# Optimization experiments

Hardware: AMD Instinct MI355X
Metric: run time of the kernel (lower is better)

The kernel has to match this reference:

```python
import jax, jax.numpy as jnp
from jax import lax
import numpy as np

T, IN, H, L = 8192, 128, 1024, 3


def setup_inputs() -> dict:
    key = jax.random.key(0)
    ks = jax.random.split(key, 12)
    s = 0.05  # scale params to avoid saturating sigmoid/tanh
    return {
        "S": jax.random.normal(ks[0], (T, IN), jnp.float32),
        "h0": jax.random.normal(ks[1], (L, H), jnp.float32),
        "w_ih0": jax.random.normal(ks[2], (2 * H, IN), jnp.float32) * s,
        "w_hh0": jax.random.normal(ks[3], (2 * H, H), jnp.float32) * s,
        "b_ih0": jax.random.normal(ks[4], (2 * H,), jnp.float32) * s,
        "b_hh0": jax.random.normal(ks[5], (2 * H,), jnp.float32) * s,
        "w_ih_rest": jax.random.normal(ks[6], (L - 1, 2 * H, H), jnp.float32) * s,
        "w_hh_rest": jax.random.normal(ks[7], (L - 1, 2 * H, H), jnp.float32) * s,
        "b_ih_rest": jax.random.normal(ks[8], (L - 1, 2 * H), jnp.float32) * s,
        "b_hh_rest": jax.random.normal(ks[9], (L - 1, 2 * H), jnp.float32) * s,
        "w_out": jax.random.normal(ks[10], (1, H), jnp.float32) * s,
        "b_out": jax.random.normal(ks[11], (1,), jnp.float32) * s,
    }


def _mgu_layer(x_seq, h0, w_ih, w_hh, b_ih, b_hh):
    # Precompute the input projection for all timesteps at once: [T, 2H]
    gi = x_seq @ w_ih.T + b_ih

    def step(h, gi_t):
        gh = h @ w_hh.T + b_hh                      # [2H]
        i_f, i_n = jnp.split(gi_t, 2)
        h_f, h_n = jnp.split(gh, 2)
        f = jax.nn.sigmoid(i_f + h_f)               # forget gate
        n = jnp.tanh(i_n + f * h_n)                 # new candidate
        hy = n + (1.0 - f) * (h - n)
        return hy, hy

    _, out = lax.scan(step, h0, gi)                 # out: [T, H]
    return out


def reference(S, h0, w_ih0, w_hh0, b_ih0, b_hh0,
              w_ih_rest, w_hh_rest, b_ih_rest, b_hh_rest,
              w_out, b_out):
    x = _mgu_layer(S, h0[0], w_ih0, w_hh0, b_ih0, b_hh0)
    for l in range(w_ih_rest.shape[0]):             # fixed small layer count
        x = _mgu_layer(x, h0[l + 1], w_ih_rest[l], w_hh_rest[l],
                       b_ih_rest[l], b_hh_rest[l])
    out = (x @ w_out.T + b_out).reshape(-1)          # [T]
    return out
```

## Files before the change

kernel.cpp:

```cpp
#include <hip/hip_runtime.h>
#include <math.h>
#include <stdint.h>


#define T_STEPS 8192
#define HDIM 1024
#define RING 128
#define SLACK (RING - 16)

typedef unsigned long long u64;

__device__ __forceinline__ u64 agload64(const u64* p) {
    return __hip_atomic_load(p, __ATOMIC_RELAXED, __HIP_MEMORY_SCOPE_AGENT);
}
__device__ __forceinline__ void agstore64(u64* p, u64 v) {
    __hip_atomic_store(p, v, __ATOMIC_RELAXED, __HIP_MEMORY_SCOPE_AGENT);
}
__device__ __forceinline__ int agloadi(const int* p) {
    return __hip_atomic_load(p, __ATOMIC_RELAXED, __HIP_MEMORY_SCOPE_AGENT);
}
__device__ __forceinline__ void agstorei(int* p, int v) {
    __hip_atomic_store(p, v, __ATOMIC_RELAXED, __HIP_MEMORY_SCOPE_AGENT);
}
__device__ __forceinline__ float dot4(float4 a, float4 b) {
    return a.x * b.x + a.y * b.y + a.z * b.z + a.w * b.w;
}
__device__ __forceinline__ u64 pack(float v, int tag) {
    return ((u64)(unsigned)tag << 32) | (u64)__float_as_uint(v);
}
__device__ __forceinline__ void opaque4(float4& v) {
    asm volatile("" : "+v"(v.x), "+v"(v.y), "+v"(v.z), "+v"(v.w));
}
__device__ __forceinline__ void opaque2(float2& v) {
    asm volatile("" : "+v"(v.x), "+v"(v.y));
}

__device__ __forceinline__ int minscan64(const int* parr, int q) {
    int p = agloadi(parr + q);
#pragma unroll
    for (int off = 32; off; off >>= 1) {
        const int o = __shfl_xor(p, off, 64);
        p = p < o ? p : o;
    }
    return p;
}

template <int L>
__device__ void rec_layer(float* __restrict__ s_h,
                          float* __restrict__ s_x0,
                          float (*__restrict__ s_gi)[16],
                          const float* __restrict__ S,
                          const float* __restrict__ h0,
                          const float* __restrict__ w_ih,
                          const float* __restrict__ b_ih,
                          const float* __restrict__ w_hh,
                          const float* __restrict__ b_hh,
                          const u64* __restrict__ giRing,
                          u64* __restrict__ ring_out,
                          float* __restrict__ xout,
                          u64* __restrict__ htag,
                          const int* __restrict__ progArr,
                          int* __restrict__ progGiSelf,
                          int r)
{
    const int tid = threadIdx.x;
    const int a   = tid >> 6;
    const int q   = tid & 63;
    const int jb  = r * 8 + 2 * a;

    float4 wf[2][4], wn[2][4];
#pragma unroll
    for (int g = 0; g < 2; ++g) {
        const float* rf = w_hh + (size_t)(jb + g) * HDIM;
        const float* rn = w_hh + (size_t)(HDIM + jb + g) * HDIM;
#pragma unroll
        for (int m = 0; m < 4; ++m) {
            wf[g][m] = *(const float4*)(rf + 4 * q + 256 * m);
            wn[g][m] = *(const float4*)(rn + 4 * q + 256 * m);
            opaque4(wf[g][m]); opaque4(wn[g][m]);
        }
    }
    float2 wif2[2] = {}, win2[2] = {};
    float bFv[2], bInv[2] = {0.f, 0.f}, bHnv[2];
    if constexpr (L == 0) {
#pragma unroll
        for (int g = 0; g < 2; ++g) {
            wif2[g] = *(const float2*)(w_ih + (size_t)(jb + g) * 128 + 2 * q);
            win2[g] = *(const float2*)(w_ih + (size_t)(HDIM + jb + g) * 128 + 2 * q);
            opaque2(wif2[g]); opaque2(win2[g]);
            bFv[g]  = b_ih[jb + g] + b_hh[jb + g];
            bInv[g] = b_ih[HDIM + jb + g];
            bHnv[g] = b_hh[HDIM + jb + g];
        }
    } else {
#pragma unroll
        for (int g = 0; g < 2; ++g) {
            bFv[g]  = b_hh[jb + g];
            bHnv[g] = b_hh[HDIM + jb + g];
        }
    }

    int lastProg = 0;

    for (int t = 0; t < T_STEPS; ++t) {
        const int par = t & 1;
        float* hD = s_h + par * HDIM;
        const u64* hrow = htag + (size_t)((t + 1) & 1) * HDIM;
        u64*       hpub = htag + (size_t)par * HDIM;

        if constexpr (L < 2) {
            if (t - lastProg > SLACK) {
                do { lastProg = minscan64(progArr, q); }
                while (t - lastProg > SLACK);
            }
        }

        if constexpr (L == 0) {
            float* xD = s_x0 + par * 128;
            if (tid < 32)
                ((float4*)xD)[tid] = ((const float4*)(S + (size_t)t * 128))[tid];
        } else {
            if (tid < 16) {
                const unsigned xe = (unsigned)(t + 1);
                const u64* p = giRing + (size_t)(t & (RING - 1)) * 2048
                             + (tid < 8 ? (size_t)(8 * r + tid)
                                        : (size_t)(1024 + 8 * r + (tid - 8)));
                u64 w;
                do { w = agload64(p); } while ((unsigned)(w >> 32) != xe);
                s_gi[par][tid] = __uint_as_float((unsigned)w);
            }
        }

        if (t == 0) {
            hD[tid]       = h0[tid];
            hD[tid + 256] = h0[tid + 256];
            hD[tid + 512] = h0[tid + 512];
            hD[tid + 768] = h0[tid + 768];
        } else {
            const unsigned he = (unsigned)t;
            u64 w0 = 0, w1 = 0, w2 = 0, w3 = 0;
            bool d0 = false, d1 = false, d2 = false, d3 = false;
            while (!(d0 && d1 && d2 && d3)) {
                if (!d0) { w0 = agload64(hrow + tid);       d0 = ((unsigned)(w0 >> 32) == he); }
                if (!d1) { w1 = agload64(hrow + tid + 256); d1 = ((unsigned)(w1 >> 32) == he); }
                if (!d2) { w2 = agload64(hrow + tid + 512); d2 = ((unsigned)(w2 >> 32) == he); }
                if (!d3) { w3 = agload64(hrow + tid + 768); d3 = ((unsigned)(w3 >> 32) == he); }
            }
            hD[tid]       = __uint_as_float((unsigned)w0);
            hD[tid + 256] = __uint_as_float((unsigned)w1);
            hD[tid + 512] = __uint_as_float((unsigned)w2);
            hD[tid + 768] = __uint_as_float((unsigned)w3);
        }
        __syncthreads();

        if constexpr (L > 0) {
            if (r == 0 && tid == 0) agstorei(progGiSelf, t + 1);
        }

        float aF[2]  = {0.f, 0.f};
        float aNh[2] = {0.f, 0.f};
        float aNi[2] = {0.f, 0.f};
#pragma unroll
        for (int m = 0; m < 4; ++m) {
            const float4 h4 = ((const float4*)hD)[q + 64 * m];
#pragma unroll
            for (int g = 0; g < 2; ++g) {
                aF[g]  += dot4(wf[g][m], h4);
                aNh[g] += dot4(wn[g][m], h4);
            }
        }
        if constexpr (L == 0) {
            const float* xD = s_x0 + par * 128;
            const float2 x2 = *(const float2*)&xD[2 * q];
#pragma unroll
            for (int g = 0; g < 2; ++g) {
                aF[g]  += wif2[g].x * x2.x + wif2[g].y * x2.y;
                aNi[g] += win2[g].x * x2.x + win2[g].y * x2.y;
            }
        }

#pragma unroll
        for (int g = 0; g < 2; ++g) {
            aF[g]  += __shfl_xor(aF[g],  1, 64);
            aNh[g] += __shfl_xor(aNh[g], 1, 64);
            if constexpr (L == 0) aNi[g] += __shfl_xor(aNi[g], 1, 64);
        }
        const int gsl = q & 1;
        float vF  = gsl ? aF[1]  : aF[0];
        float vNh = gsl ? aNh[1] : aNh[0];
        float vNi = 0.f;
        if constexpr (L == 0) vNi = gsl ? aNi[1] : aNi[0];
#pragma unroll
        for (int off = 2; off <= 32; off <<= 1) {
            vF  += __shfl_xor(vF,  off, 64);
            vNh += __shfl_xor(vNh, off, 64);
            if constexpr (L == 0) vNi += __shfl_xor(vNi, off, 64);
        }

        if (q < 2) {
            const int   j  = jb + q;
            const float hp = hD[j];
            float f, n;
            if constexpr (L == 0) {
                const float cF  = gsl ? bFv[1]  : bFv[0];
                const float cIn = gsl ? bInv[1] : bInv[0];
                const float cHn = gsl ? bHnv[1] : bHnv[0];
                f = 1.f / (1.f + expf(-(vF + cF)));
                n = tanhf(vNi + cIn + f * (vNh + cHn));
            } else {
                const float cHf = gsl ? bFv[1]  : bFv[0];
                const float cHn = gsl ? bHnv[1] : bHnv[0];
                const float gf  = s_gi[par][2 * a + q];
                const float gn  = s_gi[par][8 + 2 * a + q];
                f = 1.f / (1.f + expf(-(gf + vF + cHf)));
                n = tanhf(gn + f * (vNh + cHn));
            }
            const float hy = n + (1.f - f) * (hp - n);
            const u64   pk = pack(hy, t + 1);
            agstore64(hpub + j, pk);
            if constexpr (L < 2) {
                agstore64(ring_out + (size_t)(t & (RING - 1)) * HDIM + j, pk);
            } else {
                xout[(size_t)t * HDIM + j] = hy;
            }
        }
    }
}

__device__ void army_layer(float* __restrict__ s_x,
                           const u64* __restrict__ xring,
                           u64* __restrict__ giRing,
                           const float* __restrict__ w_ih,
                           const float* __restrict__ b_ih,
                           const int* __restrict__ progGiNext,
                           int* __restrict__ progSelf,
                           int r)
{
    const int tid = threadIdx.x;
    const int a   = tid >> 6;
    const int q   = tid & 63;
    const int jb  = r * 16 + 4 * a;

    float4 wiF[4][4], wiN[4][4];
#pragma unroll
    for (int g = 0; g < 4; ++g) {
        const float* rf = w_ih + (size_t)(jb + g) * HDIM;
        const float* rn = w_ih + (size_t)(HDIM + jb + g) * HDIM;
#pragma unroll
        for (int m = 0; m < 4; ++m) {
            wiF[g][m] = *(const float4*)(rf + 4 * q + 256 * m);
            wiN[g][m] = *(const float4*)(rn + 4 * q + 256 * m);
            opaque4(wiF[g][m]); opaque4(wiN[g][m]);
        }
    }
    float bIF[4], bIN[4];
#pragma unroll
    for (int g = 0; g < 4; ++g) {
        bIF[g] = b_ih[jb + g];
        bIN[g] = b_ih[HDIM + jb + g];
    }

    int lastProg = 0;

    for (int t = 0; t < T_STEPS; ++t) {
        const int par = t & 1;
        float* xD = s_x + par * HDIM;

        if (t - lastProg > SLACK) {
            do { lastProg = agloadi(progGiNext); } while (t - lastProg > SLACK);
        }

        {
            const unsigned xe = (unsigned)(t + 1);
            const u64* xrow = xring + (size_t)(t & (RING - 1)) * HDIM;
            u64 w0 = 0, w1 = 0, w2 = 0, w3 = 0;
            bool d0 = false, d1 = false, d2 = false, d3 = false;
            while (!(d0 && d1 && d2 && d3)) {
                if (!d0) { w0 = agload64(xrow + tid);       d0 = ((unsigned)(w0 >> 32) == xe); }
                if (!d1) { w1 = agload64(xrow + tid + 256); d1 = ((unsigned)(w1 >> 32) == xe); }
                if (!d2) { w2 = agload64(xrow + tid + 512); d2 = ((unsigned)(w2 >> 32) == xe); }
                if (!d3) { w3 = agload64(xrow + tid + 768); d3 = ((unsigned)(w3 >> 32) == xe); }
            }
            xD[tid]       = __uint_as_float((unsigned)w0);
            xD[tid + 256] = __uint_as_float((unsigned)w1);
            xD[tid + 512] = __uint_as_float((unsigned)w2);
            xD[tid + 768] = __uint_as_float((unsigned)w3);
        }
        __syncthreads();

        if (tid == 0) agstorei(progSelf, t + 1);

        float aGF[4] = {0.f, 0.f, 0.f, 0.f};
        float aGN[4] = {0.f, 0.f, 0.f, 0.f};
#pragma unroll
        for (int m = 0; m < 4; ++m) {
            const float4 x4 = ((const float4*)xD)[q + 64 * m];
#pragma unroll
            for (int g = 0; g < 4; ++g) {
                aGF[g] += dot4(wiF[g][m], x4);
                aGN[g] += dot4(wiN[g][m], x4);
            }
        }

#pragma unroll
        for (int g = 0; g < 4; ++g) {
            aGF[g] += __shfl_xor(aGF[g], 1, 64);
            aGN[g] += __shfl_xor(aGN[g], 1, 64);
        }
        const int s1 = q & 1;
        float bF0 = s1 ? aGF[1] : aGF[0];
        float bF1 = s1 ? aGF[3] : aGF[2];
        float bN0 = s1 ? aGN[1] : aGN[0];
        float bN1 = s1 ? aGN[3] : aGN[2];
        bF0 += __shfl_xor(bF0, 2, 64);
        bF1 += __shfl_xor(bF1, 2, 64);
        bN0 += __shfl_xor(bN0, 2, 64);
        bN1 += __shfl_xor(bN1, 2, 64);
        const int s2 = (q >> 1) & 1;
        float vGF = s2 ? bF1 : bF0;
        float vGN = s2 ? bN1 : bN0;
#pragma unroll
        for (int off = 4; off <= 32; off <<= 1) {
            vGF += __shfl_xor(vGF, off, 64);
            vGN += __shfl_xor(vGN, off, 64);
        }

        if (q < 4) {
            const int j = jb + q;
            u64* grow = giRing + (size_t)(t & (RING - 1)) * 2048;
            const float bf = s1 ? (s2 ? bIF[3] : bIF[1]) : (s2 ? bIF[2] : bIF[0]);
            const float bn = s1 ? (s2 ? bIN[3] : bIN[1]) : (s2 ? bIN[2] : bIN[0]);
            agstore64(grow + j,        pack(vGF + bf, t + 1));
            agstore64(grow + 1024 + j, pack(vGN + bn, t + 1));
        }
    }
}

__global__ __launch_bounds__(256, 2)
void mgu_pipe(const float* __restrict__ S,
              const float* __restrict__ h0,
              const float* __restrict__ w_ih0, const float* __restrict__ b_ih0,
              const float* __restrict__ w_hh0, const float* __restrict__ b_hh0,
              const float* __restrict__ w_ih_r, const float* __restrict__ b_ih_r,
              const float* __restrict__ w_hh_r, const float* __restrict__ b_hh_r,
              float* __restrict__ xbuf2, u64* __restrict__ ring0,
              u64* __restrict__ ring1, u64* __restrict__ gi1,
              u64* __restrict__ gi2, u64* __restrict__ htag,
              int* __restrict__ prog)
{
    __shared__ __align__(16) float s_h[2 * HDIM];
    __shared__ __align__(16) float s_x0[2 * 128];
    __shared__ float s_gi[2][16];

    int* prog_gi1 = prog + 0;
    int* prog_gi2 = prog + 16;
    int* prog_a3  = prog + 64;
    int* prog_a4  = prog + 128;

    const int bid = blockIdx.x;
    if (bid < 128) {
        rec_layer<0>(s_h, s_x0, s_gi, S, h0,
                     w_ih0, b_ih0, w_hh0, b_hh0,
                     nullptr, ring0, nullptr,
                     htag, prog_a3, nullptr, bid);
    } else if (bid < 256) {
        rec_layer<1>(s_h, nullptr, s_gi, nullptr, h0 + HDIM,
                     nullptr, nullptr, w_hh_r, b_hh_r,
                     gi1, ring1, nullptr,
                     htag + 2 * HDIM, prog_a4, prog_gi1, bid - 128);
    } else if (bid < 384) {
        rec_layer<2>(s_h, nullptr, s_gi, nullptr, h0 + 2 * HDIM,
                     nullptr, nullptr, w_hh_r + 2048 * 1024, b_hh_r + 2048,
                     gi2, nullptr, xbuf2,
                     htag + 4 * HDIM, nullptr, prog_gi2, bid - 256);
    } else if (bid < 448) {
        army_layer(s_h, ring0, gi1, w_ih_r, b_ih_r,
                   prog_gi1, prog_a3 + (bid - 384), bid - 384);
    } else {
        army_layer(s_h, ring1, gi2, w_ih_r + 2048 * 1024, b_ih_r + 2048,
                   prog_gi2, prog_a4 + (bid - 448), bid - 448);
    }
}

__global__ __launch_bounds__(256)
void mgu_out(const float* __restrict__ x,
             const float* __restrict__ w_out,
             const float* __restrict__ b_out,
             float* __restrict__ out)
{
    const int wave = threadIdx.x >> 6;
    const int lane = threadIdx.x & 63;
    const int t = blockIdx.x * 4 + wave;
    float acc = 0.f;
#pragma unroll
    for (int m = 0; m < 4; ++m) {
        const int i4 = lane + 64 * m;
        const float4 x4 = ((const float4*)(x + (size_t)t * HDIM))[i4];
        const float4 w4 = ((const float4*)w_out)[i4];
        acc += dot4(x4, w4);
    }
#pragma unroll
    for (int off = 32; off > 0; off >>= 1) acc += __shfl_xor(acc, off, 64);
    if (lane == 0) out[t] = acc + b_out[0];
}

extern "C" void kernel_launch(void* const* d_in, const int* in_sizes, int n_in,
                              void* d_out, int out_size, void* d_ws, size_t ws_size,
                              hipStream_t stream) {
    const float* S      = (const float*)d_in[0];
    const float* h0     = (const float*)d_in[1];
    const float* w_ih0  = (const float*)d_in[2];
    const float* w_hh0  = (const float*)d_in[3];
    const float* b_ih0  = (const float*)d_in[4];
    const float* b_hh0  = (const float*)d_in[5];
    const float* w_ih_r = (const float*)d_in[6];
    const float* w_hh_r = (const float*)d_in[7];
    const float* b_ih_r = (const float*)d_in[8];
    const float* b_hh_r = (const float*)d_in[9];
    const float* w_out  = (const float*)d_in[10];
    const float* b_out  = (const float*)d_in[11];
    float* out = (float*)d_out;

    char* ws = (char*)d_ws;
    float* xbuf2 = (float*)(ws);
    u64*   ring0 = (u64*)(ws + (32u << 20));
    u64*   ring1 = (u64*)(ws + (33u << 20));
    u64*   gi1   = (u64*)(ws + (34u << 20));
    u64*   gi2   = (u64*)(ws + (36u << 20));
    u64*   htag  = (u64*)(ws + (38u << 20));
    int*   prog  = (int*)(ws + (38u << 20) + (64u << 10));

    mgu_pipe<<<512, 256, 0, stream>>>(S, h0, w_ih0, b_ih0, w_hh0, b_hh0,
                                      w_ih_r, b_ih_r, w_hh_r, b_hh_r,
                                      xbuf2, ring0, ring1, gi1, gi2,
                                      htag, prog);
    mgu_out<<<2048, 256, 0, stream>>>(xbuf2, w_out, b_out, out);
}
```

Baseline: 25.07 ms.

## Repartition MGU pipeline to 512-thread blocks, 32 per layer, with sc0 polling

Each block now uses 512 threads, and blocks are interleaved by role (blockIdx & 7) so each recurrent layer runs on 32 blocks instead of 128. Each wave now computes 4 hidden units, so the per-step all-to-all h exchange has fewer participants and the progress scans cover 32 entries. The h polling uses inline-asm sc0 loads with a spin-count fallback to agent-scope atomics, and the h publish stores twice with sc0 and sc1. The gi ring load is issued before the h poll to overlap it. This risks higher per-block latency from the larger blocks and depends on cache-coherence bits that are not documented here.

```diff
diff --git a/kernel.cpp b/kernel.cpp
--- a/kernel.cpp
+++ b/kernel.cpp
@@ -7,6 +7,7 @@
 #define HDIM 1024
 #define RING 128
 #define SLACK (RING - 16)
+#define HSPIN_FB 3000
 
 typedef unsigned long long u64;
 
@@ -35,8 +36,24 @@
     asm volatile("" : "+v"(v.x), "+v"(v.y));
 }
 
-__device__ __forceinline__ int minscan64(const int* parr, int q) {
-    int p = agloadi(parr + q);
+__device__ __forceinline__ void poll2_sc0(u64& w0, u64& w1,
+                                          const u64* p0, const u64* p1) {
+    asm volatile("global_load_dwordx2 %0, %2, off sc0\n\t"
+                 "global_load_dwordx2 %1, %3, off sc0\n\t"
+                 "s_waitcnt vmcnt(0)"
+                 : "=&v"(w0), "=&v"(w1)
+                 : "v"(p0), "v"(p1)
+                 : "memory");
+    __builtin_amdgcn_sched_barrier(0);
+}
+__device__ __forceinline__ void pub_dual(u64* p, u64 v) {
+    asm volatile("global_store_dwordx2 %0, %1, off sc0\n\t"
+                 "global_store_dwordx2 %0, %1, off sc1"
+                 :: "v"(p), "v"(v) : "memory");
+}
+
+__device__ __forceinline__ int minscan32(const int* parr, int q) {
+    int p = agloadi(parr + (q & 31));
 #pragma unroll
     for (int off = 32; off; off >>= 1) {
         const int o = __shfl_xor(p, off, 64);
@@ -48,7 +65,7 @@
 template <int L>
 __device__ void rec_layer(float* __restrict__ s_h,
                           float* __restrict__ s_x0,
-                          float (*__restrict__ s_gi)[16],
+                          float (*__restrict__ s_gi)[64],
                           const float* __restrict__ S,
                           const float* __restrict__ h0,
                           const float* __restrict__ w_ih,
@@ -66,11 +83,11 @@
     const int tid = threadIdx.x;
     const int a   = tid >> 6;
     const int q   = tid & 63;
-    const int jb  = r * 8 + 2 * a;
-
-    float4 wf[2][4], wn[2][4];
-#pragma unroll
-    for (int g = 0; g < 2; ++g) {
+    const int jb  = r * 32 + 4 * a;
+
+    float4 wf[4][4], wn[4][4];
+#pragma unroll
+    for (int g = 0; g < 4; ++g) {
         const float* rf = w_hh + (size_t)(jb + g) * HDIM;
         const float* rn = w_hh + (size_t)(HDIM + jb + g) * HDIM;
 #pragma unroll
@@ -80,27 +97,25 @@
             opaque4(wf[g][m]); opaque4(wn[g][m]);
         }
     }
-    float2 wif2[2] = {}, win2[2] = {};
-    float bFv[2], bInv[2] = {0.f, 0.f}, bHnv[2];
-    if constexpr (L == 0) {
-#pragma unroll
-        for (int g = 0; g < 2; ++g) {
+    float2 wif2[4] = {}, win2[4] = {};
+    float bFv[4], bInv[4] = {}, bHnv[4];
+#pragma unroll
+    for (int g = 0; g < 4; ++g) {
+        if constexpr (L == 0) {
             wif2[g] = *(const float2*)(w_ih + (size_t)(jb + g) * 128 + 2 * q);
             win2[g] = *(const float2*)(w_ih + (size_t)(HDIM + jb + g) * 128 + 2 * q);
             opaque2(wif2[g]); opaque2(win2[g]);
             bFv[g]  = b_ih[jb + g] + b_hh[jb + g];
             bInv[g] = b_ih[HDIM + jb + g];
             bHnv[g] = b_hh[HDIM + jb + g];
-        }
-    } else {
-#pragma unroll
-        for (int g = 0; g < 2; ++g) {
+        } else {
             bFv[g]  = b_hh[jb + g];
             bHnv[g] = b_hh[HDIM + jb + g];
         }
     }
 
-    int lastProg = 0;
+    int  lastProg = 0;
+    bool hslow    = false;
 
     for (int t = 0; t < T_STEPS; ++t) {
         const int par = t & 1;
@@ -110,46 +125,63 @@
 
         if constexpr (L < 2) {
             if (t - lastProg > SLACK) {
-                do { lastProg = minscan64(progArr, q); }
+                do { lastProg = minscan32(progArr, q); }
                 while (t - lastProg > SLACK);
             }
         }
 
-        if constexpr (L == 0) {
-            float* xD = s_x0 + par * 128;
+        float4 sv;
+        u64 gw = 0; const u64* gp = nullptr;
+        if constexpr (L == 0) {
             if (tid < 32)
-                ((float4*)xD)[tid] = ((const float4*)(S + (size_t)t * 128))[tid];
+                sv = ((const float4*)(S + (size_t)t * 128))[tid];
         } else {
-            if (tid < 16) {
-                const unsigned xe = (unsigned)(t + 1);
-                const u64* p = giRing + (size_t)(t & (RING - 1)) * 2048
-                             + (tid < 8 ? (size_t)(8 * r + tid)
-                                        : (size_t)(1024 + 8 * r + (tid - 8)));
-                u64 w;
-                do { w = agload64(p); } while ((unsigned)(w >> 32) != xe);
-                s_gi[par][tid] = __uint_as_float((unsigned)w);
+            if (tid < 64) {
+                gp = giRing + (size_t)(t & (RING - 1)) * 2048
+                   + (tid < 32 ? (size_t)(32 * r + tid)
+                               : (size_t)(1024 + 32 * r + (tid - 32)));
+                gw = agload64(gp);
             }
         }
 
         if (t == 0) {
             hD[tid]       = h0[tid];
-            hD[tid + 256] = h0[tid + 256];
             hD[tid + 512] = h0[tid + 512];
-            hD[tid + 768] = h0[tid + 768];
         } else {
             const unsigned he = (unsigned)t;
-            u64 w0 = 0, w1 = 0, w2 = 0, w3 = 0;
-            bool d0 = false, d1 = false, d2 = false, d3 = false;
-            while (!(d0 && d1 && d2 && d3)) {
-                if (!d0) { w0 = agload64(hrow + tid);       d0 = ((unsigned)(w0 >> 32) == he); }
-                if (!d1) { w1 = agload64(hrow + tid + 256); d1 = ((unsigned)(w1 >> 32) == he); }
-                if (!d2) { w2 = agload64(hrow + tid + 512); d2 = ((unsigned)(w2 >> 32) == he); }
-                if (!d3) { w3 = agload64(hrow + tid + 768); d3 = ((unsigned)(w3 >> 32) == he); }
-            }
-            hD[tid]       = __uint_as_float((unsigned)w0);
-            hD[tid + 256] = __uint_as_float((unsigned)w1);
-            hD[tid + 512] = __uint_as_float((unsigned)w2);
-            hD[tid + 768] = __uint_as_float((unsigned)w3);
+            const u64* p0 = hrow + tid;
+            const u64* p1 = hrow + tid + 512;
+            u64 hw0 = 0, hw1 = 0;
+            bool done = false;
+            if (!hslow) {
+                int spins = 0;
+                for (;;) {
+                    poll2_sc0(hw0, hw1, p0, p1);
+                    if ((unsigned)(hw0 >> 32) == he &&
+                        (unsigned)(hw1 >> 32) == he) { done = true; break; }
+                    if (++spins > HSPIN_FB) { hslow = true; break; }
+                }
+            }
+            if (!done) {
+                bool d0 = ((unsigned)(hw0 >> 32) == he);
+                bool d1 = ((unsigned)(hw1 >> 32) == he);
+                while (!(d0 && d1)) {
+                    if (!d0) { hw0 = agload64(p0); d0 = ((unsigned)(hw0 >> 32) == he); }
+                    if (!d1) { hw1 = agload64(p1); d1 = ((unsigned)(hw1 >> 32) == he); }
+                }
+            }
+            hD[tid]       = __uint_as_float((unsigned)hw0);
+            hD[tid + 512] = __uint_as_float((unsigned)hw1);
+        }
+
+        if constexpr (L == 0) {
+            if (tid < 32) ((float4*)(s_x0 + par * 128))[tid] = sv;
+        } else {
+            if (tid < 64) {
+                const unsigned xe = (unsigned)(t + 1);
+                while ((unsigned)(gw >> 32) != xe) gw = agload64(gp);
+                s_gi[par][tid] = __uint_as_float((unsigned)gw);
+            }
         }
         __syncthreads();
 
@@ -157,14 +189,14 @@
             if (r == 0 && tid == 0) agstorei(progGiSelf, t + 1);
         }
 
-        float aF[2]  = {0.f, 0.f};
-        float aNh[2] = {0.f, 0.f};
-        float aNi[2] = {0.f, 0.f};
+        float aF[4]  = {};
+        float aNh[4] = {};
+        float aNi[4] = {};
 #pragma unroll
         for (int m = 0; m < 4; ++m) {
             const float4 h4 = ((const float4*)hD)[q + 64 * m];
 #pragma unroll
-            for (int g = 0; g < 2; ++g) {
+            for (int g = 0; g < 4; ++g) {
                 aF[g]  += dot4(wf[g][m], h4);
                 aNh[g] += dot4(wn[g][m], h4);
             }
@@ -173,51 +205,67 @@
             const float* xD = s_x0 + par * 128;
             const float2 x2 = *(const float2*)&xD[2 * q];
 #pragma unroll
-            for (int g = 0; g < 2; ++g) {
+            for (int g = 0; g < 4; ++g) {
                 aF[g]  += wif2[g].x * x2.x + wif2[g].y * x2.y;
                 aNi[g] += win2[g].x * x2.x + win2[g].y * x2.y;
             }
         }
 
 #pragma unroll
-        for (int g = 0; g < 2; ++g) {
+        for (int g = 0; g < 4; ++g) {
             aF[g]  += __shfl_xor(aF[g],  1, 64);
             aNh[g] += __shfl_xor(aNh[g], 1, 64);
             if constexpr (L == 0) aNi[g] += __shfl_xor(aNi[g], 1, 64);
         }
-        const int gsl = q & 1;
-        float vF  = gsl ? aF[1]  : aF[0];
-        float vNh = gsl ? aNh[1] : aNh[0];
+        const int s1 = q & 1;
+        float fF0  = s1 ? aF[1]  : aF[0];
+        float fF1  = s1 ? aF[3]  : aF[2];
+        float fNh0 = s1 ? aNh[1] : aNh[0];
+        float fNh1 = s1 ? aNh[3] : aNh[2];
+        float fNi0 = 0.f, fNi1 = 0.f;
+        if constexpr (L == 0) {
+            fNi0 = s1 ? aNi[1] : aNi[0];
+            fNi1 = s1 ? aNi[3] : aNi[2];
+        }
+        fF0  += __shfl_xor(fF0,  2, 64);
+        fF1  += __shfl_xor(fF1,  2, 64);
+        fNh0 += __shfl_xor(fNh0, 2, 64);
+        fNh1 += __shfl_xor(fNh1, 2, 64);
+        if constexpr (L == 0) {
+            fNi0 += __shfl_xor(fNi0, 2, 64);
+            fNi1 += __shfl_xor(fNi1, 2, 64);
+        }
+        const int s2 = (q >> 1) & 1;
+        float vF  = s2 ? fF1  : fF0;
+        float vNh = s2 ? fNh1 : fNh0;
         float vNi = 0.f;
-        if constexpr (L == 0) vNi = gsl ? aNi[1] : aNi[0];
-#pragma unroll
-        for (int off = 2; off <= 32; off <<= 1) {
+        if constexpr (L == 0) vNi = s2 ? fNi1 : fNi0;
+#pragma unroll
+        for (int off = 4; off <= 32; off <<= 1) {
             vF  += __shfl_xor(vF,  off, 64);
             vNh += __shfl_xor(vNh, off, 64);
             if constexpr (L == 0) vNi += __shfl_xor(vNi, off, 64);
         }
 
-        if (q < 2) {
+        if (q < 4) {
             const int   j  = jb + q;
             const float hp = hD[j];
+            const float cF  = s1 ? (s2 ? bFv[3]  : bFv[1])  : (s2 ? bFv[2]  : bFv[0]);
+            const float cHn = s1 ? (s2 ? bHnv[3] : bHnv[1]) : (s2 ? bHnv[2] : bHnv[0]);
             float f, n;
             if constexpr (L == 0) {
-                const float cF  = gsl ? bFv[1]  : bFv[0];
-                const float cIn = gsl ? bInv[1] : bInv[0];
-                const float cHn = gsl ? bHnv[1] : bHnv[0];
+                const float cIn = s1 ? (s2 ? bInv[3] : bInv[1]) : (s2 ? bInv[2] : bInv[0]);
                 f = 1.f / (1.f + expf(-(vF + cF)));
                 n = tanhf(vNi + cIn + f * (vNh + cHn));
             } else {
-                const float cHf = gsl ? bFv[1]  : bFv[0];
-                const float cHn = gsl ? bHnv[1] : bHnv[0];
-                const float gf  = s_gi[par][2 * a + q];
-                const float gn  = s_gi[par][8 + 2 * a + q];
-                f = 1.f / (1.f + expf(-(gf + vF + cHf)));
+                const float gf = s_gi[par][4 * a + q];
+                const float gn = s_gi[par][32 + 4 * a + q];
+                f = 1.f / (1.f + expf(-(gf + vF + cF)));
                 n = tanhf(gn + f * (vNh + cHn));
             }
             const float hy = n + (1.f - f) * (hp - n);
             const u64   pk = pack(hy, t + 1);
-            agstore64(hpub + j, pk);
+            pub_dual(hpub + j, pk);
             if constexpr (L < 2) {
                 agstore64(ring_out + (size_t)(t & (RING - 1)) * HDIM + j, pk);
             } else {
@@ -239,7 +287,7 @@
     const int tid = threadIdx.x;
     const int a   = tid >> 6;
     const int q   = tid & 63;
-    const int jb  = r * 16 + 4 * a;
+    const int jb  = r * 32 + 4 * a;
 
     float4 wiF[4][4], wiN[4][4];
 #pragma unroll
@@ -273,25 +321,21 @@
         {
             const unsigned xe = (unsigned)(t + 1);
             const u64* xrow = xring + (size_t)(t & (RING - 1)) * HDIM;
-            u64 w0 = 0, w1 = 0, w2 = 0, w3 = 0;
-            bool d0 = false, d1 = false, d2 = false, d3 = false;
-            while (!(d0 && d1 && d2 && d3)) {
+            u64 w0 = 0, w1 = 0;
+            bool d0 = false, d1 = false;
+            while (!(d0 && d1)) {
                 if (!d0) { w0 = agload64(xrow + tid);       d0 = ((unsigned)(w0 >> 32) == xe); }
-                if (!d1) { w1 = agload64(xrow + tid + 256); d1 = ((unsigned)(w1 >> 32) == xe); }
-                if (!d2) { w2 = agload64(xrow + tid + 512); d2 = ((unsigned)(w2 >> 32) == xe); }
-                if (!d3) { w3 = agload64(xrow + tid + 768); d3 = ((unsigned)(w3 >> 32) == xe); }
+                if (!d1) { w1 = agload64(xrow + tid + 512); d1 = ((unsigned)(w1 >> 32) == xe); }
             }
             xD[tid]       = __uint_as_float((unsigned)w0);
-            xD[tid + 256] = __uint_as_float((unsigned)w1);
-            xD[tid + 512] = __uint_as_float((unsigned)w2);
-            xD[tid + 768] = __uint_as_float((unsigned)w3);
+            xD[tid + 512] = __uint_as_float((unsigned)w1);
         }
         __syncthreads();
 
         if (tid == 0) agstorei(progSelf, t + 1);
 
-        float aGF[4] = {0.f, 0.f, 0.f, 0.f};
-        float aGN[4] = {0.f, 0.f, 0.f, 0.f};
+        float aGF[4] = {};
+        float aGN[4] = {};
 #pragma unroll
         for (int m = 0; m < 4; ++m) {
             const float4 x4 = ((const float4*)xD)[q + 64 * m];
@@ -336,7 +380,7 @@
     }
 }
 
-__global__ __launch_bounds__(256, 2)
+__global__ __launch_bounds__(512, 2)
 void mgu_pipe(const float* __restrict__ S,
               const float* __restrict__ h0,
               const float* __restrict__ w_ih0, const float* __restrict__ b_ih0,
@@ -350,35 +394,38 @@
 {
     __shared__ __align__(16) float s_h[2 * HDIM];
     __shared__ __align__(16) float s_x0[2 * 128];
-    __shared__ float s_gi[2][16];
+    __shared__ float s_gi[2][64];
 
     int* prog_gi1 = prog + 0;
     int* prog_gi2 = prog + 16;
-    int* prog_a3  = prog + 64;
-    int* prog_a4  = prog + 128;
-
-    const int bid = blockIdx.x;
-    if (bid < 128) {
+    int* prog_a1  = prog + 64;
+    int* prog_a2  = prog + 128;
+
+    const int role = blockIdx.x & 7;
+    const int r    = blockIdx.x >> 3;
+    if (r >= 32) return;
+
+    if (role == 0) {
         rec_layer<0>(s_h, s_x0, s_gi, S, h0,
                      w_ih0, b_ih0, w_hh0, b_hh0,
                      nullptr, ring0, nullptr,
-                     htag, prog_a3, nullptr, bid);
-    } else if (bid < 256) {
+                     htag, prog_a1, nullptr, r);
+    } else if (role == 1) {
         rec_layer<1>(s_h, nullptr, s_gi, nullptr, h0 + HDIM,
                      nullptr, nullptr, w_hh_r, b_hh_r,
                      gi1, ring1, nullptr,
-                     htag + 2 * HDIM, prog_a4, prog_gi1, bid - 128);
-    } else if (bid < 384) {
+                     htag + 2 * HDIM, prog_a2, prog_gi1, r);
+    } else if (role == 2) {
         rec_layer<2>(s_h, nullptr, s_gi, nullptr, h0 + 2 * HDIM,
                      nullptr, nullptr, w_hh_r + 2048 * 1024, b_hh_r + 2048,
                      gi2, nullptr, xbuf2,
-                     htag + 4 * HDIM, nullptr, prog_gi2, bid - 256);
-    } else if (bid < 448) {
+                     htag + 4 * HDIM, nullptr, prog_gi2, r);
+    } else if (role == 3) {
         army_layer(s_h, ring0, gi1, w_ih_r, b_ih_r,
-                   prog_gi1, prog_a3 + (bid - 384), bid - 384);
-    } else {
+                   prog_gi1, prog_a1 + r, r);
+    } else if (role == 4) {
         army_layer(s_h, ring1, gi2, w_ih_r + 2048 * 1024, b_ih_r + 2048,
-                   prog_gi2, prog_a4 + (bid - 448), bid - 448);
+                   prog_gi2, prog_a2 + r, r);
     }
 }
 
@@ -430,7 +477,7 @@
     u64*   htag  = (u64*)(ws + (38u << 20));
     int*   prog  = (int*)(ws + (38u << 20) + (64u << 10));
 
-    mgu_pipe<<<512, 256, 0, stream>>>(S, h0, w_ih0, b_ih0, w_hh0, b_hh0,
+    mgu_pipe<<<512, 512, 0, stream>>>(S, h0, w_ih0, b_ih0, w_hh0, b_hh0,
                                       w_ih_r, b_ih_r, w_hh_r, b_hh_r,
                                       xbuf2, ring0, ring1, gi1, gi2,
                                       htag, prog);
```

Result: slower. 38.50 ms (+53.6%).

## Repartition persistent MGU pipeline into fewer fatter blocks with dual-path h publishing

Applied to the files above, without the earlier changes.

Each recurrent block now owns 32 hidden units (8 per wave) instead of 8, so each layer spans 32 blocks and 256 blocks launch with one block per CU. Blocks are interleaved by role across the grid. The hidden state is published to two buffers, one through L2-scoped stores and one through a second cache-policy store, and readers poll the L2 copy first, then fall back to the other with a sticky switch. Gate-input loads are issued early and waited on after the h poll. The aim is fewer blocks in each per-step barrier and lower sync latency, at the cost of much higher register pressure (8x4 float4 weights per gate) and fewer threads sharing each step's work.

```diff
diff --git a/kernel.cpp b/kernel.cpp
--- a/kernel.cpp
+++ b/kernel.cpp
@@ -7,6 +7,8 @@
 #define HDIM 1024
 #define RING 128
 #define SLACK (RING - 16)
+#define FBH 12
+#define STICKY 8
 
 typedef unsigned long long u64;
 
@@ -35,8 +37,27 @@
     asm volatile("" : "+v"(v.x), "+v"(v.y));
 }
 
-__device__ __forceinline__ int minscan64(const int* parr, int q) {
-    int p = agloadi(parr + q);
+__device__ __forceinline__ void poll4_sc0(u64& w0, u64& w1, u64& w2, u64& w3,
+                                          const u64* p0, const u64* p1,
+                                          const u64* p2, const u64* p3) {
+    asm volatile("global_load_dwordx2 %0, %4, off sc0\n\t"
+                 "global_load_dwordx2 %1, %5, off sc0\n\t"
+                 "global_load_dwordx2 %2, %6, off sc0\n\t"
+                 "global_load_dwordx2 %3, %7, off sc0\n\t"
+                 "s_waitcnt vmcnt(0)"
+                 : "=&v"(w0), "=&v"(w1), "=&v"(w2), "=&v"(w3)
+                 : "v"(p0), "v"(p1), "v"(p2), "v"(p3)
+                 : "memory");
+    __builtin_amdgcn_sched_barrier(0);
+}
+__device__ __forceinline__ void pub_dual(u64* pl2, u64* pml, u64 v) {
+    asm volatile("global_store_dwordx2 %0, %2, off sc0\n\t"
+                 "global_store_dwordx2 %1, %2, off sc1"
+                 :: "v"(pl2), "v"(pml), "v"(v) : "memory");
+}
+
+__device__ __forceinline__ int minscan32(const int* parr, int q) {
+    int p = agloadi(parr + (q & 31));
 #pragma unroll
     for (int off = 32; off; off >>= 1) {
         const int o = __shfl_xor(p, off, 64);
@@ -45,10 +66,20 @@
     return p;
 }
 
+__device__ __forceinline__ float sel8(const float (&b)[8], int s1, int s2, int s4) {
+    const float e0 = s1 ? b[1] : b[0];
+    const float e1 = s1 ? b[3] : b[2];
+    const float e2 = s1 ? b[5] : b[4];
+    const float e3 = s1 ? b[7] : b[6];
+    const float f0 = s2 ? e1 : e0;
+    const float f1 = s2 ? e3 : e2;
+    return s4 ? f1 : f0;
+}
+
 template <int L>
 __device__ void rec_layer(float* __restrict__ s_h,
                           float* __restrict__ s_x0,
-                          float (*__restrict__ s_gi)[16],
+                          float* __restrict__ s_gi,
                           const float* __restrict__ S,
                           const float* __restrict__ h0,
                           const float* __restrict__ w_ih,
@@ -58,7 +89,8 @@
                           const u64* __restrict__ giRing,
                           u64* __restrict__ ring_out,
                           float* __restrict__ xout,
-                          u64* __restrict__ htag,
+                          u64* __restrict__ hl2,
+                          u64* __restrict__ hml,
                           const int* __restrict__ progArr,
                           int* __restrict__ progGiSelf,
                           int r)
@@ -66,11 +98,11 @@
     const int tid = threadIdx.x;
     const int a   = tid >> 6;
     const int q   = tid & 63;
-    const int jb  = r * 8 + 2 * a;
-
-    float4 wf[2][4], wn[2][4];
-#pragma unroll
-    for (int g = 0; g < 2; ++g) {
+    const int jb  = r * 32 + 8 * a;
+
+    float4 wf[8][4], wn[8][4];
+#pragma unroll
+    for (int g = 0; g < 8; ++g) {
         const float* rf = w_hh + (size_t)(jb + g) * HDIM;
         const float* rn = w_hh + (size_t)(HDIM + jb + g) * HDIM;
 #pragma unroll
@@ -80,54 +112,53 @@
             opaque4(wf[g][m]); opaque4(wn[g][m]);
         }
     }
-    float2 wif2[2] = {}, win2[2] = {};
-    float bFv[2], bInv[2] = {0.f, 0.f}, bHnv[2];
-    if constexpr (L == 0) {
-#pragma unroll
-        for (int g = 0; g < 2; ++g) {
+    float2 wif2[8] = {}, win2[8] = {};
+    float bFv[8], bInv[8] = {}, bHnv[8];
+#pragma unroll
+    for (int g = 0; g < 8; ++g) {
+        if constexpr (L == 0) {
             wif2[g] = *(const float2*)(w_ih + (size_t)(jb + g) * 128 + 2 * q);
             win2[g] = *(const float2*)(w_ih + (size_t)(HDIM + jb + g) * 128 + 2 * q);
             opaque2(wif2[g]); opaque2(win2[g]);
             bFv[g]  = b_ih[jb + g] + b_hh[jb + g];
             bInv[g] = b_ih[HDIM + jb + g];
             bHnv[g] = b_hh[HDIM + jb + g];
-        }
-    } else {
-#pragma unroll
-        for (int g = 0; g < 2; ++g) {
+        } else {
             bFv[g]  = b_hh[jb + g];
             bHnv[g] = b_hh[HDIM + jb + g];
         }
     }
 
-    int lastProg = 0;
+    int  lastProg   = 0;
+    int  failStreak = 0;
+    bool hslow      = false;
 
     for (int t = 0; t < T_STEPS; ++t) {
-        const int par = t & 1;
+        const int par   = t & 1;
+        const int rdpar = (t + 1) & 1;
         float* hD = s_h + par * HDIM;
-        const u64* hrow = htag + (size_t)((t + 1) & 1) * HDIM;
-        u64*       hpub = htag + (size_t)par * HDIM;
+        const u64* hrowL2 = hl2 + (size_t)rdpar * HDIM;
+        const u64* hrowML = hml + (size_t)rdpar * HDIM;
+        u64*       hpubL2 = hl2 + (size_t)par * HDIM;
+        u64*       hpubML = hml + (size_t)par * HDIM;
 
         if constexpr (L < 2) {
             if (t - lastProg > SLACK) {
-                do { lastProg = minscan64(progArr, q); }
+                do { lastProg = minscan32(progArr, q); }
                 while (t - lastProg > SLACK);
             }
         }
 
+        float4 sv = {};
+        u64 gw = 0; const u64* gp = nullptr;
         if constexpr (L == 0) {
-            float* xD = s_x0 + par * 128;
-            if (tid < 32)
-                ((float4*)xD)[tid] = ((const float4*)(S + (size_t)t * 128))[tid];
+            if (tid < 32) sv = ((const float4*)(S + (size_t)t * 128))[tid];
         } else {
-            if (tid < 16) {
-                const unsigned xe = (unsigned)(t + 1);
-                const u64* p = giRing + (size_t)(t & (RING - 1)) * 2048
-                             + (tid < 8 ? (size_t)(8 * r + tid)
-                                        : (size_t)(1024 + 8 * r + (tid - 8)));
-                u64 w;
-                do { w = agload64(p); } while ((unsigned)(w >> 32) != xe);
-                s_gi[par][tid] = __uint_as_float((unsigned)w);
+            if (tid < 64) {
+                gp = giRing + (size_t)(t & (RING - 1)) * 2048
+                   + (tid < 32 ? (size_t)(32 * r + tid)
+                               : (size_t)(1024 + 32 * r + (tid - 32)));
+                gw = agload64(gp);
             }
         }
 
@@ -138,33 +169,69 @@
             hD[tid + 768] = h0[tid + 768];
         } else {
             const unsigned he = (unsigned)t;
+            const u64 *p0 = hrowL2 + tid,       *p1 = hrowL2 + tid + 256,
+                      *p2 = hrowL2 + tid + 512, *p3 = hrowL2 + tid + 768;
+            const u64 *m0 = hrowML + tid,       *m1 = hrowML + tid + 256,
+                      *m2 = hrowML + tid + 512, *m3 = hrowML + tid + 768;
             u64 w0 = 0, w1 = 0, w2 = 0, w3 = 0;
-            bool d0 = false, d1 = false, d2 = false, d3 = false;
-            while (!(d0 && d1 && d2 && d3)) {
-                if (!d0) { w0 = agload64(hrow + tid);       d0 = ((unsigned)(w0 >> 32) == he); }
-                if (!d1) { w1 = agload64(hrow + tid + 256); d1 = ((unsigned)(w1 >> 32) == he); }
-                if (!d2) { w2 = agload64(hrow + tid + 512); d2 = ((unsigned)(w2 >> 32) == he); }
-                if (!d3) { w3 = agload64(hrow + tid + 768); d3 = ((unsigned)(w3 >> 32) == he); }
+            bool hok = false;
+            if (!hslow) {
+                int rounds = 0;
+                do {
+                    poll4_sc0(w0, w1, w2, w3, p0, p1, p2, p3);
+                    hok = ((unsigned)(w0 >> 32) == he) &&
+                          ((unsigned)(w1 >> 32) == he) &&
+                          ((unsigned)(w2 >> 32) == he) &&
+                          ((unsigned)(w3 >> 32) == he);
+                } while (!hok && ++rounds < FBH);
+            }
+            if (!hok) {
+                bool d0 = ((unsigned)(w0 >> 32) == he);
+                bool d1 = ((unsigned)(w1 >> 32) == he);
+                bool d2 = ((unsigned)(w2 >> 32) == he);
+                bool d3 = ((unsigned)(w3 >> 32) == he);
+                int iters = 0;
+                while (!(d0 && d1 && d2 && d3)) {
+                    ++iters;
+                    if (!d0) { w0 = agload64(m0); d0 = ((unsigned)(w0 >> 32) == he); }
+                    if (!d1) { w1 = agload64(m1); d1 = ((unsigned)(w1 >> 32) == he); }
+                    if (!d2) { w2 = agload64(m2); d2 = ((unsigned)(w2 >> 32) == he); }
+                    if (!d3) { w3 = agload64(m3); d3 = ((unsigned)(w3 >> 32) == he); }
+                }
+                if (!hslow) {
+                    if (iters <= 2) { if (++failStreak >= STICKY) hslow = true; }
+                    else failStreak = 0;
+                }
+            } else {
+                failStreak = 0;
             }
             hD[tid]       = __uint_as_float((unsigned)w0);
             hD[tid + 256] = __uint_as_float((unsigned)w1);
             hD[tid + 512] = __uint_as_float((unsigned)w2);
             hD[tid + 768] = __uint_as_float((unsigned)w3);
         }
+
+        if constexpr (L == 0) {
+            if (tid < 32) ((float4*)(s_x0 + par * 128))[tid] = sv;
+        } else {
+            if (tid < 64) {
+                const unsigned xe = (unsigned)(t + 1);
+                while ((unsigned)(gw >> 32) != xe) gw = agload64(gp);
+                s_gi[par * 64 + tid] = __uint_as_float((unsigned)gw);
+            }
+        }
         __syncthreads();
 
         if constexpr (L > 0) {
             if (r == 0 && tid == 0) agstorei(progGiSelf, t + 1);
         }
 
-        float aF[2]  = {0.f, 0.f};
-        float aNh[2] = {0.f, 0.f};
-        float aNi[2] = {0.f, 0.f};
+        float aF[8] = {}, aNh[8] = {}, aNi[8] = {};
 #pragma unroll
         for (int m = 0; m < 4; ++m) {
             const float4 h4 = ((const float4*)hD)[q + 64 * m];
 #pragma unroll
-            for (int g = 0; g < 2; ++g) {
+            for (int g = 0; g < 8; ++g) {
                 aF[g]  += dot4(wf[g][m], h4);
                 aNh[g] += dot4(wn[g][m], h4);
             }
@@ -173,55 +240,83 @@
             const float* xD = s_x0 + par * 128;
             const float2 x2 = *(const float2*)&xD[2 * q];
 #pragma unroll
-            for (int g = 0; g < 2; ++g) {
+            for (int g = 0; g < 8; ++g) {
                 aF[g]  += wif2[g].x * x2.x + wif2[g].y * x2.y;
                 aNi[g] += win2[g].x * x2.x + win2[g].y * x2.y;
             }
         }
 
-#pragma unroll
-        for (int g = 0; g < 2; ++g) {
+        const int s1 = q & 1, s2 = (q >> 1) & 1, s4 = (q >> 2) & 1;
+#pragma unroll
+        for (int g = 0; g < 8; ++g) {
             aF[g]  += __shfl_xor(aF[g],  1, 64);
             aNh[g] += __shfl_xor(aNh[g], 1, 64);
             if constexpr (L == 0) aNi[g] += __shfl_xor(aNi[g], 1, 64);
         }
-        const int gsl = q & 1;
-        float vF  = gsl ? aF[1]  : aF[0];
-        float vNh = gsl ? aNh[1] : aNh[0];
+        float bF[4], bNh[4], bNi[4] = {};
+#pragma unroll
+        for (int g2 = 0; g2 < 4; ++g2) {
+            bF[g2]  = s1 ? aF[2 * g2 + 1]  : aF[2 * g2];
+            bNh[g2] = s1 ? aNh[2 * g2 + 1] : aNh[2 * g2];
+            if constexpr (L == 0) bNi[g2] = s1 ? aNi[2 * g2 + 1] : aNi[2 * g2];
+        }
+#pragma unroll
+        for (int g2 = 0; g2 < 4; ++g2) {
+            bF[g2]  += __shfl_xor(bF[g2],  2, 64);
+            bNh[g2] += __shfl_xor(bNh[g2], 2, 64);
+            if constexpr (L == 0) bNi[g2] += __shfl_xor(bNi[g2], 2, 64);
+        }
+        float cF[2], cNh[2], cNi[2] = {};
+#pragma unroll
+        for (int g4 = 0; g4 < 2; ++g4) {
+            cF[g4]  = s2 ? bF[2 * g4 + 1]  : bF[2 * g4];
+            cNh[g4] = s2 ? bNh[2 * g4 + 1] : bNh[2 * g4];
+            if constexpr (L == 0) cNi[g4] = s2 ? bNi[2 * g4 + 1] : bNi[2 * g4];
+        }
+#pragma unroll
+        for (int g4 = 0; g4 < 2; ++g4) {
+            cF[g4]  += __shfl_xor(cF[g4],  4, 64);
+            cNh[g4] += __shfl_xor(cNh[g4], 4, 64);
+            if constexpr (L == 0) cNi[g4] += __shfl_xor(cNi[g4], 4, 64);
+        }
+        float vF  = s4 ? cF[1]  : cF[0];
+        float vNh = s4 ? cNh[1] : cNh[0];
         float vNi = 0.f;
-        if constexpr (L == 0) vNi = gsl ? aNi[1] : aNi[0];
-#pragma unroll
-        for (int off = 2; off <= 32; off <<= 1) {
+        if constexpr (L == 0) vNi = s4 ? cNi[1] : cNi[0];
+#pragma unroll
+        for (int off = 8; off <= 32; off <<= 1) {
             vF  += __shfl_xor(vF,  off, 64);
             vNh += __shfl_xor(vNh, off, 64);
             if constexpr (L == 0) vNi += __shfl_xor(vNi, off, 64);
         }
 
-        if (q < 2) {
-            const int   j  = jb + q;
+        {
+            const int   ju = q & 7;
+            const int   j  = jb + ju;
             const float hp = hD[j];
+            const float cFb  = sel8(bFv,  s1, s2, s4);
+            const float cHnb = sel8(bHnv, s1, s2, s4);
             float f, n;
             if constexpr (L == 0) {
-                const float cF  = gsl ? bFv[1]  : bFv[0];
-                const float cIn = gsl ? bInv[1] : bInv[0];
-                const float cHn = gsl ? bHnv[1] : bHnv[0];
-                f = 1.f / (1.f + expf(-(vF + cF)));
-                n = tanhf(vNi + cIn + f * (vNh + cHn));
+                const float cInb = sel8(bInv, s1, s2, s4);
+                f = 1.f / (1.f + expf(-(vF + cFb)));
+                n = tanhf(vNi + cInb + f * (vNh + cHnb));
             } else {
-                const float cHf = gsl ? bFv[1]  : bFv[0];
-                const float cHn = gsl ? bHnv[1] : bHnv[0];
-                const float gf  = s_gi[par][2 * a + q];
-                const float gn  = s_gi[par][8 + 2 * a + q];
-                f = 1.f / (1.f + expf(-(gf + vF + cHf)));
-                n = tanhf(gn + f * (vNh + cHn));
+                const int u = 8 * a + ju;
+                const float gf = s_gi[par * 64 + u];
+                const float gn = s_gi[par * 64 + 32 + u];
+                f = 1.f / (1.f + expf(-(gf + vF + cFb)));
+                n = tanhf(gn + f * (vNh + cHnb));
             }
             const float hy = n + (1.f - f) * (hp - n);
-            const u64   pk = pack(hy, t + 1);
-            agstore64(hpub + j, pk);
-            if constexpr (L < 2) {
-                agstore64(ring_out + (size_t)(t & (RING - 1)) * HDIM + j, pk);
-            } else {
-                xout[(size_t)t * HDIM + j] = hy;
+            if (q < 8) {
+                const u64 pk = pack(hy, t + 1);
+                pub_dual(hpubL2 + j, hpubML + j, pk);
+                if constexpr (L < 2) {
+                    agstore64(ring_out + (size_t)(t & (RING - 1)) * HDIM + j, pk);
+                } else {
+                    xout[(size_t)t * HDIM + j] = hy;
+                }
             }
         }
     }
@@ -239,11 +334,11 @@
     const int tid = threadIdx.x;
     const int a   = tid >> 6;
     const int q   = tid & 63;
-    const int jb  = r * 16 + 4 * a;
-
-    float4 wiF[4][4], wiN[4][4];
-#pragma unroll
-    for (int g = 0; g < 4; ++g) {
+    const int jb  = r * 32 + 8 * a;
+
+    float4 wiF[8][4], wiN[8][4];
+#pragma unroll
+    for (int g = 0; g < 8; ++g) {
         const float* rf = w_ih + (size_t)(jb + g) * HDIM;
         const float* rn = w_ih + (size_t)(HDIM + jb + g) * HDIM;
 #pragma unroll
@@ -253,9 +348,9 @@
             opaque4(wiF[g][m]); opaque4(wiN[g][m]);
         }
     }
-    float bIF[4], bIN[4];
-#pragma unroll
-    for (int g = 0; g < 4; ++g) {
+    float bIF[8], bIN[8];
+#pragma unroll
+    for (int g = 0; g < 8; ++g) {
         bIF[g] = b_ih[jb + g];
         bIN[g] = b_ih[HDIM + jb + g];
     }
@@ -290,53 +385,65 @@
 
         if (tid == 0) agstorei(progSelf, t + 1);
 
-        float aGF[4] = {0.f, 0.f, 0.f, 0.f};
-        float aGN[4] = {0.f, 0.f, 0.f, 0.f};
+        float aGF[8] = {}, aGN[8] = {};
 #pragma unroll
         for (int m = 0; m < 4; ++m) {
             const float4 x4 = ((const float4*)xD)[q + 64 * m];
 #pragma unroll
-            for (int g = 0; g < 4; ++g) {
+            for (int g = 0; g < 8; ++g) {
                 aGF[g] += dot4(wiF[g][m], x4);
                 aGN[g] += dot4(wiN[g][m], x4);
             }
         }
 
-#pragma unroll
-        for (int g = 0; g < 4; ++g) {
+        const int s1 = q & 1, s2 = (q >> 1) & 1, s4 = (q >> 2) & 1;
+#pragma unroll
+        for (int g = 0; g < 8; ++g) {
             aGF[g] += __shfl_xor(aGF[g], 1, 64);
             aGN[g] += __shfl_xor(aGN[g], 1, 64);
         }
-        const int s1 = q & 1;
-        float bF0 = s1 ? aGF[1] : aGF[0];
-        float bF1 = s1 ? aGF[3] : aGF[2];
-        float bN0 = s1 ? aGN[1] : aGN[0];
-        float bN1 = s1 ? aGN[3] : aGN[2];
-        bF0 += __shfl_xor(bF0, 2, 64);
-        bF1 += __shfl_xor(bF1, 2, 64);
-        bN0 += __shfl_xor(bN0, 2, 64);
-        bN1 += __shfl_xor(bN1, 2, 64);
-        const int s2 = (q >> 1) & 1;
-        float vGF = s2 ? bF1 : bF0;
-        float vGN = s2 ? bN1 : bN0;
-#pragma unroll
-        for (int off = 4; off <= 32; off <<= 1) {
+        float bF[4], bN[4];
+#pragma unroll
+        for (int g2 = 0; g2 < 4; ++g2) {
+            bF[g2] = s1 ? aGF[2 * g2 + 1] : aGF[2 * g2];
+            bN[g2] = s1 ? aGN[2 * g2 + 1] : aGN[2 * g2];
+        }
+#pragma unroll
+        for (int g2 = 0; g2 < 4; ++g2) {
+            bF[g2] += __shfl_xor(bF[g2], 2, 64);
+            bN[g2] += __shfl_xor(bN[g2], 2, 64);
+        }
+        float cFv[2], cNv[2];
+#pragma unroll
+        for (int g4 = 0; g4 < 2; ++g4) {
+            cFv[g4] = s2 ? bF[2 * g4 + 1] : bF[2 * g4];
+            cNv[g4] = s2 ? bN[2 * g4 + 1] : bN[2 * g4];
+        }
+#pragma unroll
+        for (int g4 = 0; g4 < 2; ++g4) {
+            cFv[g4] += __shfl_xor(cFv[g4], 4, 64);
+            cNv[g4] += __shfl_xor(cNv[g4], 4, 64);
+        }
+        float vGF = s4 ? cFv[1] : cFv[0];
+        float vGN = s4 ? cNv[1] : cNv[0];
+#pragma unroll
+        for (int off = 8; off <= 32; off <<= 1) {
             vGF += __shfl_xor(vGF, off, 64);
             vGN += __shfl_xor(vGN, off, 64);
         }
 
-        if (q < 4) {
+        if (q < 8) {
             const int j = jb + q;
             u64* grow = giRing + (size_t)(t & (RING - 1)) * 2048;
-            const float bf = s1 ? (s2 ? bIF[3] : bIF[1]) : (s2 ? bIF[2] : bIF[0]);
-            const float bn = s1 ? (s2 ? bIN[3] : bIN[1]) : (s2 ? bIN[2] : bIN[0]);
+            const float bf = sel8(bIF, s1, s2, s4);
+            const float bn = sel8(bIN, s1, s2, s4);
             agstore64(grow + j,        pack(vGF + bf, t + 1));
             agstore64(grow + 1024 + j, pack(vGN + bn, t + 1));
         }
     }
 }
 
-__global__ __launch_bounds__(256, 2)
+__global__ __launch_bounds__(256, 1)
 void mgu_pipe(const float* __restrict__ S,
               const float* __restrict__ h0,
               const float* __restrict__ w_ih0, const float* __restrict__ b_ih0,
@@ -345,40 +452,44 @@
               const float* __restrict__ w_hh_r, const float* __restrict__ b_hh_r,
               float* __restrict__ xbuf2, u64* __restrict__ ring0,
               u64* __restrict__ ring1, u64* __restrict__ gi1,
-              u64* __restrict__ gi2, u64* __restrict__ htag,
-              int* __restrict__ prog)
+              u64* __restrict__ gi2, u64* __restrict__ hl2,
+              u64* __restrict__ hml, int* __restrict__ prog)
 {
-    __shared__ __align__(16) float s_h[2 * HDIM];
+    __shared__ __align__(16) float s_main[2 * HDIM];
     __shared__ __align__(16) float s_x0[2 * 128];
-    __shared__ float s_gi[2][16];
+    __shared__ float s_gi[2 * 64];
 
     int* prog_gi1 = prog + 0;
     int* prog_gi2 = prog + 16;
-    int* prog_a3  = prog + 64;
-    int* prog_a4  = prog + 128;
-
-    const int bid = blockIdx.x;
-    if (bid < 128) {
-        rec_layer<0>(s_h, s_x0, s_gi, S, h0,
+    int* prog_a1  = prog + 64;
+    int* prog_a2  = prog + 128;
+
+    const int role = blockIdx.x & 7;
+    const int r    = blockIdx.x >> 3;
+
+    if (role == 0) {
+        rec_layer<0>(s_main, s_x0, s_gi, S, h0,
                      w_ih0, b_ih0, w_hh0, b_hh0,
                      nullptr, ring0, nullptr,
-                     htag, prog_a3, nullptr, bid);
-    } else if (bid < 256) {
-        rec_layer<1>(s_h, nullptr, s_gi, nullptr, h0 + HDIM,
+                     hl2, hml, prog_a1, nullptr, r);
+    } else if (role == 1) {
+        rec_layer<1>(s_main, nullptr, s_gi, nullptr, h0 + HDIM,
                      nullptr, nullptr, w_hh_r, b_hh_r,
                      gi1, ring1, nullptr,
-                     htag + 2 * HDIM, prog_a4, prog_gi1, bid - 128);
-    } else if (bid < 384) {
-        rec_layer<2>(s_h, nullptr, s_gi, nullptr, h0 + 2 * HDIM,
+                     hl2 + 2 * HDIM, hml + 2 * HDIM,
+                     prog_a2, prog_gi1, r);
+    } else if (role == 2) {
+        rec_layer<2>(s_main, nullptr, s_gi, nullptr, h0 + 2 * HDIM,
                      nullptr, nullptr, w_hh_r + 2048 * 1024, b_hh_r + 2048,
                      gi2, nullptr, xbuf2,
-                     htag + 4 * HDIM, nullptr, prog_gi2, bid - 256);
-    } else if (bid < 448) {
-        army_layer(s_h, ring0, gi1, w_ih_r, b_ih_r,
-                   prog_gi1, prog_a3 + (bid - 384), bid - 384);
-    } else {
-        army_layer(s_h, ring1, gi2, w_ih_r + 2048 * 1024, b_ih_r + 2048,
-                   prog_gi2, prog_a4 + (bid - 448), bid - 448);
+                     hl2 + 4 * HDIM, hml + 4 * HDIM,
+                     nullptr, prog_gi2, r);
+    } else if (role == 3) {
+        army_layer(s_main, ring0, gi1, w_ih_r, b_ih_r,
+                   prog_gi1, prog_a1 + r, r);
+    } else if (role == 4) {
+        army_layer(s_main, ring1, gi2, w_ih_r + 2048 * 1024, b_ih_r + 2048,
+                   prog_gi2, prog_a2 + r, r);
     }
 }
 
@@ -427,12 +538,13 @@
     u64*   ring1 = (u64*)(ws + (33u << 20));
     u64*   gi1   = (u64*)(ws + (34u << 20));
     u64*   gi2   = (u64*)(ws + (36u << 20));
-    u64*   htag  = (u64*)(ws + (38u << 20));
-    int*   prog  = (int*)(ws + (38u << 20) + (64u << 10));
-
-    mgu_pipe<<<512, 256, 0, stream>>>(S, h0, w_ih0, b_ih0, w_hh0, b_hh0,
+    u64*   hl2   = (u64*)(ws + (38u << 20));
+    u64*   hml   = (u64*)(ws + (38u << 20) + (64u << 10));
+    int*   prog  = (int*)(ws + (38u << 20) + (128u << 10));
+
+    mgu_pipe<<<256, 256, 0, stream>>>(S, h0, w_ih0, b_ih0, w_hh0, b_hh0,
                                       w_ih_r, b_ih_r, w_hh_r, b_hh_r,
                                       xbuf2, ring0, ring1, gi1, gi2,
-                                      htag, prog);
+                                      hl2, hml, prog);
     mgu_out<<<2048, 256, 0, stream>>>(xbuf2, w_out, b_out, out);
 }
```

New measurement: 47.99 ms. 91.4% more time.
